# Kernel optimization log

Measured on AMD Instinct MI355X. Metric: run time of the kernel, lower is better.

Reference implementation:

```python
import jax, jax.numpy as jnp
import numpy as np
from jax import lax

# QConv2d: conv2d implemented in the original via unfold + quantized matmul
# with a dequantization scale. High-precision path math:
#   out = scale * conv2d(x, weight) + bias
# We express the im2col+GEMM as the mathematically identical conv.

STRIDE = (1, 1)
PADDING = ((1, 1), (1, 1))


def setup_inputs() -> dict:
    key = jax.random.key(0)
    k1, k2, k3 = jax.random.split(key, 3)
    N, C, H, W = 16, 32, 256, 256
    O, KH, KW = 32, 3, 3
    x = jax.random.normal(k1, (N, C, H, W), dtype=jnp.float32)
    weight = jax.random.normal(k2, (O, C, KH, KW), dtype=jnp.float32) * 0.1
    bias = jax.random.normal(k3, (O,), dtype=jnp.float32)
    scale = jnp.float32(0.0078125)  # quantization dequant scale (1/128)
    return {"x": x, "weight": weight, "bias": bias, "scale": scale}


def reference(x, weight, bias, scale):
    # conv2d (NCHW / OIHW), stride 1, padding 1 -> same spatial size
    out = lax.conv_general_dilated(
        x, weight,
        window_strides=STRIDE,
        padding=PADDING,
        dimension_numbers=("NCHW", "OIHW", "NCHW"),
    )
    # scale applied by the quantized matmul kernel, then bias
    return out * scale + bias[None, :, None, None]
```

## Files before the change

### kernel.cpp

```cpp
#include <hip/hip_runtime.h>

typedef unsigned short u16;
typedef unsigned int   u32;
typedef short s8v  __attribute__((ext_vector_type(8)));
typedef float f16v __attribute__((ext_vector_type(16)));

#define ROWBYTES 4224
#define NROWS    18
#define LDS_BYTES (NROWS * ROWBYTES)

__device__ inline u16 f2bf(float f) {
    u32 u = __builtin_bit_cast(u32, f);
    u += 0x7FFFu + ((u >> 16) & 1u);
    return (u16)(u >> 16);
}
__device__ inline u32 pk2(float lo, float hi) {
    return (u32)f2bf(lo) | ((u32)f2bf(hi) << 16);
}

__global__ __launch_bounds__(256, 2) void k_fused(const float* __restrict__ x,
                                                  const float* __restrict__ wgt,
                                                  const float* __restrict__ bias,
                                                  const float* __restrict__ scale_p,
                                                  float* __restrict__ out) {
    __shared__ __align__(16) char lds[LDS_BYTES];

    const int b    = blockIdx.x;
    const int wb   = b & 3;
    const int hs   = (b >> 2) & 15;
    const int n    = b >> 6;
    const int w0   = wb << 6;
    const int h0   = hs << 4;
    const int t    = threadIdx.x;
    const int l    = t & 63;
    const int wave = t >> 6;
    const int g    = l >> 5;
    const int ln   = l & 31;

    {
        u16* wl = (u16*)lds;
        #pragma unroll
        for (int k = 0; k < 36; ++k) {
            const int idx = t + (k << 8);
            const int tap = idx % 9;
            const int oc  = idx / 9;
            wl[tap * 1024 + oc] = f2bf(wgt[idx]);
        }
    }
    __syncthreads();

    s8v A[9][2];
    {
        const u16* wl = (const u16*)lds;
        #pragma unroll
        for (int tap = 0; tap < 9; ++tap)
            #pragma unroll
            for (int q = 0; q < 2; ++q)
                A[tap][q] = *(const s8v*)(wl + tap * 1024 + ln * 32 + q * 16 + g * 8);
    }
    const float scale = scale_p[0];
    float bias_r[16];
    #pragma unroll
    for (int rg = 0; rg < 16; ++rg) bias_r[rg] = bias[(rg & 3) + 8 * (rg >> 2) + 4 * g];
    __syncthreads();

    const float* xbase = x + ((size_t)n << 21);
    for (int r = 0; r < NROWS; ++r) {
        const int hin = h0 - 1 + r;
        const bool hv = (hin >= 0) && (hin < 256);
        const float* xrow = xbase + (size_t)hin * 256;
        char* lrow = lds + r * ROWBYTES;
        #pragma unroll
        for (int k = 0; k < 2; ++k) {
            const int idx = t + (k << 8);
            const int cp  = idx >> 5;
            const int ph  = idx & 31;
            float2 va{0.f, 0.f}, vb{0.f, 0.f};
            if (hv) {
                const float* p = xrow + cp * 131072 + w0 + (ph << 1);
                va = *(const float2*)p;
                vb = *(const float2*)(p + 65536);
            }
            char* dst = lrow + (cp >> 2) * 1056 + ((1 + (ph << 1)) << 4) + ((cp & 3) << 2);
            *(u32*)dst        = pk2(va.x, vb.x);
            *(u32*)(dst + 16) = pk2(va.y, vb.y);
        }
    }
    for (int idx = t; idx < 576; idx += 256) {
        const int r    = idx >> 5;
        const int side = (idx >> 4) & 1;
        const int cp   = idx & 15;
        const int hin  = h0 - 1 + r;
        const int wg   = w0 - 1 + side * 65;
        float a = 0.f, c2 = 0.f;
        if (hin >= 0 && hin < 256 && wg >= 0 && wg < 256) {
            const float* p = xbase + (size_t)hin * 256 + cp * 131072 + wg;
            a  = p[0];
            c2 = p[65536];
        }
        *(u32*)(lds + r * ROWBYTES + (cp >> 2) * 1056 + side * 1040 + ((cp & 3) << 2)) = pk2(a, c2);
    }
    __syncthreads();

    #pragma unroll
    for (int i = 0; i < 4; ++i) {
        const int hr = (wave << 2) + i;

        f16v acc0, acc1;
        #pragma unroll
        for (int rg = 0; rg < 16; ++rg) { acc0[rg] = 0.f; acc1[rg] = 0.f; }

        #pragma unroll
        for (int kh = 0; kh < 3; ++kh) {
            const char* rowp = lds + (hr + kh) * ROWBYTES + g * 1056 + (ln << 4);
            #pragma unroll
            for (int kw = 0; kw < 3; ++kw) {
                const int tap = kh * 3 + kw;
                #pragma unroll
                for (int q = 0; q < 2; ++q) {
                    const char* pB = rowp + q * 2112 + (kw << 4);
                    const s8v b0 = *(const s8v*)pB;
                    const s8v b1 = *(const s8v*)(pB + 512);
                    acc0 = __builtin_amdgcn_mfma_f32_32x32x16_bf16(A[tap][q], b0, acc0, 0, 0, 0);
                    acc1 = __builtin_amdgcn_mfma_f32_32x32x16_bf16(A[tap][q], b1, acc1, 0, 0, 0);
                }
            }
        }

        const int h = h0 + hr;
        float* op = out + ((size_t)n << 21) + (size_t)h * 256 + w0 + ln;
        #pragma unroll
        for (int rg = 0; rg < 16; ++rg) {
            const int o = (rg & 3) + 8 * (rg >> 2) + 4 * g;
            op[(size_t)o * 65536]      = scale * acc0[rg] + bias_r[rg];
            op[(size_t)o * 65536 + 32] = scale * acc1[rg] + bias_r[rg];
        }
    }
}

extern "C" void kernel_launch(void* const* d_in, const int* in_sizes, int n_in,
                              void* d_out, int out_size, void* d_ws, size_t ws_size,
                              hipStream_t stream) {
    const float* x     = (const float*)d_in[0];
    const float* wgt   = (const float*)d_in[1];
    const float* bias  = (const float*)d_in[2];
    const float* scale = (const float*)d_in[3];
    float* out = (float*)d_out;
    k_fused<<<dim3(1024), dim3(256), 0, stream>>>(x, wgt, bias, scale, out);
}
```

Baseline: 67.63 us.

## Halve row tile, restructure LDS fill with 8-channel vector stores, nontemporal output

```diff
diff --git a/kernel.cpp b/kernel.cpp
--- a/kernel.cpp
+++ b/kernel.cpp
@@ -4,9 +4,10 @@
 typedef unsigned int   u32;
 typedef short s8v  __attribute__((ext_vector_type(8)));
 typedef float f16v __attribute__((ext_vector_type(16)));
+typedef unsigned int u32x4 __attribute__((ext_vector_type(4)));
 
 #define ROWBYTES 4224
-#define NROWS    18
+#define NROWS    10
 #define LDS_BYTES (NROWS * ROWBYTES)
 
 __device__ inline u16 f2bf(float f) {
@@ -18,7 +19,7 @@
     return (u32)f2bf(lo) | ((u32)f2bf(hi) << 16);
 }
 
-__global__ __launch_bounds__(256, 2) void k_fused(const float* __restrict__ x,
+__global__ __launch_bounds__(256, 3) void k_fused(const float* __restrict__ x,
                                                   const float* __restrict__ wgt,
                                                   const float* __restrict__ bias,
                                                   const float* __restrict__ scale_p,
@@ -27,10 +28,10 @@
 
     const int b    = blockIdx.x;
     const int wb   = b & 3;
-    const int hs   = (b >> 2) & 15;
-    const int n    = b >> 6;
+    const int hs   = (b >> 2) & 31;
+    const int n    = b >> 7;
     const int w0   = wb << 6;
-    const int h0   = hs << 4;
+    const int h0   = hs << 3;
     const int t    = threadIdx.x;
     const int l    = t & 63;
     const int wave = t >> 6;
@@ -65,46 +66,45 @@
     __syncthreads();
 
     const float* xbase = x + ((size_t)n << 21);
-    for (int r = 0; r < NROWS; ++r) {
-        const int hin = h0 - 1 + r;
-        const bool hv = (hin >= 0) && (hin < 256);
-        const float* xrow = xbase + (size_t)hin * 256;
-        char* lrow = lds + r * ROWBYTES;
-        #pragma unroll
-        for (int k = 0; k < 2; ++k) {
-            const int idx = t + (k << 8);
-            const int cp  = idx >> 5;
-            const int ph  = idx & 31;
-            float2 va{0.f, 0.f}, vb{0.f, 0.f};
-            if (hv) {
-                const float* p = xrow + cp * 131072 + w0 + (ph << 1);
-                va = *(const float2*)p;
-                vb = *(const float2*)(p + 65536);
-            }
-            char* dst = lrow + (cp >> 2) * 1056 + ((1 + (ph << 1)) << 4) + ((cp & 3) << 2);
-            *(u32*)dst        = pk2(va.x, vb.x);
-            *(u32*)(dst + 16) = pk2(va.y, vb.y);
-        }
-    }
-    for (int idx = t; idx < 576; idx += 256) {
-        const int r    = idx >> 5;
-        const int side = (idx >> 4) & 1;
-        const int cp   = idx & 15;
+
+    if (t < 80) {
+        const int r    = t % 10;
+        const int side = (t / 10) & 1;
+        const int cc   = t / 20;
         const int hin  = h0 - 1 + r;
         const int wg   = w0 - 1 + side * 65;
-        float a = 0.f, c2 = 0.f;
+        u32 q0 = 0, q1 = 0, q2 = 0, q3 = 0;
         if (hin >= 0 && hin < 256 && wg >= 0 && wg < 256) {
-            const float* p = xbase + (size_t)hin * 256 + cp * 131072 + wg;
-            a  = p[0];
-            c2 = p[65536];
+            const float* p = xbase + (size_t)(cc * 8) * 65536 + (size_t)hin * 256 + wg;
+            q0 = pk2(p[0],      p[65536]);
+            q1 = pk2(p[131072], p[196608]);
+            q2 = pk2(p[262144], p[327680]);
+            q3 = pk2(p[393216], p[458752]);
         }
-        *(u32*)(lds + r * ROWBYTES + (cp >> 2) * 1056 + side * 1040 + ((cp & 3) << 2)) = pk2(a, c2);
+        *(u32x4*)(lds + r * ROWBYTES + cc * 1056 + side * 1040) = u32x4{q0, q1, q2, q3};
+    }
+
+    {
+        const float* pb = xbase + (size_t)(wave * 8) * 65536 + w0 + l;
+        char* ldst = lds + wave * 1056 + ((l + 1) << 4);
+        #pragma unroll
+        for (int r = 0; r < NROWS; ++r) {
+            const int hin = h0 - 1 + r;
+            u32 q0 = 0, q1 = 0, q2 = 0, q3 = 0;
+            if (hin >= 0 && hin < 256) {
+                const float* p = pb + (size_t)hin * 256;
+                const float c0 = p[0],      c1 = p[65536],  c2 = p[131072], c3 = p[196608];
+                const float c4 = p[262144], c5 = p[327680], c6 = p[393216], c7 = p[458752];
+                q0 = pk2(c0, c1); q1 = pk2(c2, c3); q2 = pk2(c4, c5); q3 = pk2(c6, c7);
+            }
+            *(u32x4*)(ldst + r * ROWBYTES) = u32x4{q0, q1, q2, q3};
+        }
     }
     __syncthreads();
 
     #pragma unroll
-    for (int i = 0; i < 4; ++i) {
-        const int hr = (wave << 2) + i;
+    for (int i = 0; i < 2; ++i) {
+        const int hr = (wave << 1) + i;
 
         f16v acc0, acc1;
         #pragma unroll
@@ -132,8 +132,8 @@
         #pragma unroll
         for (int rg = 0; rg < 16; ++rg) {
             const int o = (rg & 3) + 8 * (rg >> 2) + 4 * g;
-            op[(size_t)o * 65536]      = scale * acc0[rg] + bias_r[rg];
-            op[(size_t)o * 65536 + 32] = scale * acc1[rg] + bias_r[rg];
+            __builtin_nontemporal_store(scale * acc0[rg] + bias_r[rg], op + (size_t)o * 65536);
+            __builtin_nontemporal_store(scale * acc1[rg] + bias_r[rg], op + (size_t)o * 65536 + 32);
         }
     }
 }
@@ -146,5 +146,5 @@
     const float* bias  = (const float*)d_in[2];
     const float* scale = (const float*)d_in[3];
     float* out = (float*)d_out;
-    k_fused<<<dim3(1024), dim3(256), 0, stream>>>(x, wgt, bias, scale, out);
+    k_fused<<<dim3(2048), dim3(256), 0, stream>>>(x, wgt, bias, scale, out);
 }
```

New measurement: 72.81 us. 1.08x slower.
